# Optimization experiments

Hardware: AMD Instinct MI355X
Metric: run time of the kernel (lower is better)

## Reference

```python
import jax, jax.numpy as jnp
import numpy as np

VOCAB = 100000
DIM = 128
B = 16384
K = 20


def setup_inputs() -> dict:
    key = jax.random.key(0)
    k1, k2, k3, k4, k5 = jax.random.split(key, 5)
    return {
        "target": jax.random.randint(k1, (B,), 0, VOCAB),
        "context": jax.random.randint(k2, (B,), 0, VOCAB),
        "neg_samples": jax.random.randint(k3, (B, K), 0, VOCAB),
        "in_embed": jax.random.normal(k4, (VOCAB, DIM), dtype=jnp.float32),
        "out_embed": jax.random.normal(k5, (VOCAB, DIM), dtype=jnp.float32),
    }


def reference(target, context, neg_samples, in_embed, out_embed):
    t = in_embed[target]            # [B, D]
    c = out_embed[context]          # [B, D]
    n = out_embed[neg_samples]      # [B, K, D]

    pos_score = jnp.einsum("bd,bd->b", t, c)          # [B]
    pos_loss = jax.nn.log_sigmoid(pos_score)           # [B]

    neg_score = jnp.einsum("bd,bkd->bk", t, n)        # [B, K]
    neg_loss = jax.nn.log_sigmoid(-neg_score).sum(axis=1)  # [B]

    # Original torch broadcasts pos_loss[B] + neg_loss[B,1] -> [B,B] then .mean();
    # that equals mean(pos_loss) + mean(neg_loss), computed here without the [B,B].
    return -(pos_loss.mean() + neg_loss.mean())
```

## Files before the change

kernel.cpp:

```cpp
#include <hip/hip_runtime.h>
#include <hip/hip_bf16.h>

#define VOCAB 100000
#define DIM   128
#define BATCH 16384
#define KNEG  20

__global__ __launch_bounds__(256) void skipgram_loss_kernel(
    const int*   __restrict__ target,
    const int*   __restrict__ context,
    const int*   __restrict__ neg_samples,
    const float* __restrict__ in_embed,
    const float* __restrict__ out_embed,
    float*       __restrict__ out)
{
    const int lane  = threadIdx.x & 63;
    const int half  = lane >> 5;
    const int sub   = lane & 31;
    const int wave  = threadIdx.x >> 6;
    const int wpb   = blockDim.x >> 6;
    const int gwave = blockIdx.x * wpb + wave;
    const int nwav  = gridDim.x * wpb;

    float acc = 0.0f;

    for (int b0 = gwave * 2; b0 < BATCH; b0 += nwav * 2) {
        const int b    = b0 + half;
        const int trow = target[b];
        const int crow = context[b];

        const float4 t4 = *(const float4*)(in_embed  + (size_t)trow * DIM + sub * 4);
        const float4 c4 = *(const float4*)(out_embed + (size_t)crow * DIM + sub * 4);

        const int myidx = (sub < KNEG) ? neg_samples[b * KNEG + sub] : 0;

        int nrow[KNEG];
        #pragma unroll
        for (int k = 0; k < KNEG; ++k)
            nrow[k] = __shfl(myidx, k, 32);

        float p[KNEG + 1];
        p[0] = t4.x * c4.x + t4.y * c4.y + t4.z * c4.z + t4.w * c4.w;

        #pragma unroll
        for (int k = 0; k < KNEG; ++k) {
            const float4 n4 = *(const float4*)(out_embed + (size_t)nrow[k] * DIM + sub * 4);
            p[k + 1] = t4.x * n4.x + t4.y * n4.y + t4.z * n4.z + t4.w * n4.w;
        }

        #pragma unroll
        for (int k = 0; k < KNEG + 1; ++k) {
            float v = p[k];
            #pragma unroll
            for (int m = 1; m < 32; m <<= 1)
                v += __shfl_xor(v, m, 64);
            const float x  = (k == 0) ? v : -v;
            const float ls = fminf(x, 0.0f) - __logf(1.0f + __expf(-fabsf(x)));
            acc += ls;
        }
    }

    __shared__ float smem[8];
    if (sub == 0) smem[wave * 2 + half] = acc;
    __syncthreads();
    if (threadIdx.x == 0) {
        float tot = 0.0f;
        for (int i = 0; i < wpb * 2; ++i) tot += smem[i];
        atomicAdd(out, -tot * (1.0f / (float)BATCH));
    }
}

extern "C" void kernel_launch(void* const* d_in, const int* in_sizes, int n_in,
                              void* d_out, int out_size, void* d_ws, size_t ws_size,
                              hipStream_t stream) {
    const int*   target      = (const int*)  d_in[0];
    const int*   context     = (const int*)  d_in[1];
    const int*   neg_samples = (const int*)  d_in[2];
    const float* in_embed    = (const float*)d_in[3];
    const float* out_embed   = (const float*)d_in[4];
    float*       out         = (float*)d_out;

    hipMemsetAsync(out, 0, sizeof(float), stream);

    skipgram_loss_kernel<<<2048, 256, 0, stream>>>(
        target, context, neg_samples, in_embed, out_embed, out);
}
```

Measured before the change: 145.3 us.

## Invert negative-sample gather into per-vocab-row bucket traversal with bf16 targets

Replaces the per-batch gather of 20 random out_embed rows with a two-pass scheme. The first pass buckets negative samples by vocabulary row using atomic counters, fixed slots and an overflow list. It also computes the positive loss and writes target rows as bf16. The second pass streams each used out_embed row once and dots it against the bf16 target rows. This aims to cut repeated random fp32 reads of the large table, at the cost of atomics, extra kernels and memsets, and lower precision for the target vectors. Overflow is capped, so extreme collisions could silently drop terms.

```diff
diff --git a/kernel.cpp b/kernel.cpp
--- a/kernel.cpp
+++ b/kernel.cpp
@@ -5,59 +5,138 @@
 #define DIM   128
 #define BATCH 16384
 #define KNEG  20
-
-__global__ __launch_bounds__(256) void skipgram_loss_kernel(
+#define NNEG  (BATCH * KNEG)
+#define CAP   16
+#define OVF_CAP 65536
+
+#define CNT_OFF   0ul
+#define OVFC_OFF  400000ul
+#define SLOT_OFF  400064ul
+#define TBF_OFF   3600128ul
+#define OVF_OFF   7794432ul
+#define WS_NEED   (OVF_OFF + OVF_CAP * 4ul)
+
+typedef float v4f __attribute__((ext_vector_type(4)));
+
+__device__ __forceinline__ unsigned short f2bf(float f) {
+    unsigned u = __float_as_uint(f);
+    return (unsigned short)((u + 0x7fffu + ((u >> 16) & 1u)) >> 16);
+}
+__device__ __forceinline__ float bf2f(unsigned short u) {
+    return __uint_as_float(((unsigned)u) << 16);
+}
+__device__ __forceinline__ float log_sigmoid(float x) {
+    return fminf(x, 0.0f) - __logf(1.0f + __expf(-fabsf(x)));
+}
+
+__global__ __launch_bounds__(256) void scatter_pos_kernel(
     const int*   __restrict__ target,
     const int*   __restrict__ context,
     const int*   __restrict__ neg_samples,
     const float* __restrict__ in_embed,
     const float* __restrict__ out_embed,
-    float*       __restrict__ out)
+    unsigned*       cnt, unsigned* ovfc,
+    unsigned short* slots, unsigned short* tbf, unsigned* ovf,
+    float* __restrict__ out)
+{
+    if (blockIdx.x < 1280) {
+        const int i = blockIdx.x * 256 + threadIdx.x;
+        const int b = i / KNEG;
+        const int r = neg_samples[i];
+        const unsigned pos = atomicAdd(&cnt[r], 1u);
+        if (pos < CAP) {
+            slots[r * CAP + pos] = (unsigned short)b;
+        } else {
+            const unsigned o = atomicAdd(ovfc, 1u);
+            if (o < OVF_CAP) ovf[o] = ((unsigned)r << 14) | (unsigned)b;
+        }
+        return;
+    }
+    const int blk  = blockIdx.x - 1280;
+    const int lane = threadIdx.x & 63;
+    const int half = lane >> 5;
+    const int sub  = lane & 31;
+    const int wave = threadIdx.x >> 6;
+    const int b    = blk * 8 + wave * 2 + half;
+
+    const int trow = target[b];
+    const int crow = context[b];
+    const float4 t4 = *(const float4*)(in_embed  + (size_t)trow * DIM + sub * 4);
+    const float4 c4 = *(const float4*)(out_embed + (size_t)crow * DIM + sub * 4);
+
+    ushort4 u;
+    u.x = f2bf(t4.x); u.y = f2bf(t4.y); u.z = f2bf(t4.z); u.w = f2bf(t4.w);
+    *(ushort4*)(tbf + (size_t)b * DIM + sub * 4) = u;
+
+    float v = t4.x * c4.x + t4.y * c4.y + t4.z * c4.z + t4.w * c4.w;
+    #pragma unroll
+    for (int m = 1; m < 32; m <<= 1) v += __shfl_xor(v, m, 64);
+    const float ls = log_sigmoid(v);
+
+    __shared__ float smem[8];
+    if (sub == 0) smem[wave * 2 + half] = ls;
+    __syncthreads();
+    if (threadIdx.x == 0) {
+        float tot = 0.0f;
+        #pragma unroll
+        for (int j = 0; j < 8; ++j) tot += smem[j];
+        atomicAdd(out, -tot * (1.0f / (float)BATCH));
+    }
+}
+
+__global__ __launch_bounds__(256) void neg_rows_kernel(
+    const float* __restrict__ out_embed,
+    const unsigned* __restrict__ cnt, const unsigned* __restrict__ ovfc,
+    const unsigned short* __restrict__ slots,
+    const unsigned short* __restrict__ tbf,
+    const unsigned* __restrict__ ovf,
+    float* __restrict__ out)
 {
     const int lane  = threadIdx.x & 63;
     const int half  = lane >> 5;
     const int sub   = lane & 31;
     const int wave  = threadIdx.x >> 6;
-    const int wpb   = blockDim.x >> 6;
-    const int gwave = blockIdx.x * wpb + wave;
-    const int nwav  = gridDim.x * wpb;
+    const int ghalf = (blockIdx.x * 4 + wave) * 2 + half;
+    const int nhalf = gridDim.x * 8;
 
     float acc = 0.0f;
 
-    for (int b0 = gwave * 2; b0 < BATCH; b0 += nwav * 2) {
-        const int b    = b0 + half;
-        const int trow = target[b];
-        const int crow = context[b];
-
-        const float4 t4 = *(const float4*)(in_embed  + (size_t)trow * DIM + sub * 4);
-        const float4 c4 = *(const float4*)(out_embed + (size_t)crow * DIM + sub * 4);
-
-        const int myidx = (sub < KNEG) ? neg_samples[b * KNEG + sub] : 0;
-
-        int nrow[KNEG];
-        #pragma unroll
-        for (int k = 0; k < KNEG; ++k)
-            nrow[k] = __shfl(myidx, k, 32);
-
-        float p[KNEG + 1];
-        p[0] = t4.x * c4.x + t4.y * c4.y + t4.z * c4.z + t4.w * c4.w;
-
-        #pragma unroll
-        for (int k = 0; k < KNEG; ++k) {
-            const float4 n4 = *(const float4*)(out_embed + (size_t)nrow[k] * DIM + sub * 4);
-            p[k + 1] = t4.x * n4.x + t4.y * n4.y + t4.z * n4.z + t4.w * n4.w;
-        }
-
-        #pragma unroll
-        for (int k = 0; k < KNEG + 1; ++k) {
-            float v = p[k];
+    for (int r = ghalf; r < VOCAB; r += nhalf) {
+        const unsigned c = __builtin_nontemporal_load(&cnt[r]);
+        if (c == 0) continue;
+
+        const v4f o4 = __builtin_nontemporal_load(
+            (const v4f*)(out_embed + (size_t)r * DIM + sub * 4));
+
+        const int m = (c < CAP) ? (int)c : CAP;
+        for (int j = 0; j < m; ++j) {
+            const int b = __builtin_nontemporal_load(&slots[r * CAP + j]);
+            const uint2 tu = *(const uint2*)(tbf + (size_t)b * DIM + sub * 4);
+            float p = o4.x * bf2f((unsigned short)(tu.x & 0xffff))
+                    + o4.y * bf2f((unsigned short)(tu.x >> 16))
+                    + o4.z * bf2f((unsigned short)(tu.y & 0xffff))
+                    + o4.w * bf2f((unsigned short)(tu.y >> 16));
             #pragma unroll
-            for (int m = 1; m < 32; m <<= 1)
-                v += __shfl_xor(v, m, 64);
-            const float x  = (k == 0) ? v : -v;
-            const float ls = fminf(x, 0.0f) - __logf(1.0f + __expf(-fabsf(x)));
-            acc += ls;
-        }
+            for (int s = 1; s < 32; s <<= 1) p += __shfl_xor(p, s, 64);
+            acc += log_sigmoid(-p);
+        }
+    }
+
+    unsigned novf = *ovfc;
+    if (novf > OVF_CAP) novf = OVF_CAP;
+    for (unsigned i = ghalf; i < novf; i += nhalf) {
+        const unsigned e = ovf[i];
+        const int r = (int)(e >> 14);
+        const int b = (int)(e & 16383u);
+        const float4 o4 = *(const float4*)(out_embed + (size_t)r * DIM + sub * 4);
+        const uint2 tu = *(const uint2*)(tbf + (size_t)b * DIM + sub * 4);
+        float p = o4.x * bf2f((unsigned short)(tu.x & 0xffff))
+                + o4.y * bf2f((unsigned short)(tu.x >> 16))
+                + o4.z * bf2f((unsigned short)(tu.y & 0xffff))
+                + o4.w * bf2f((unsigned short)(tu.y >> 16));
+        #pragma unroll
+        for (int s = 1; s < 32; s <<= 1) p += __shfl_xor(p, s, 64);
+        acc += log_sigmoid(-p);
     }
 
     __shared__ float smem[8];
@@ -65,7 +144,52 @@
     __syncthreads();
     if (threadIdx.x == 0) {
         float tot = 0.0f;
-        for (int i = 0; i < wpb * 2; ++i) tot += smem[i];
+        #pragma unroll
+        for (int j = 0; j < 8; ++j) tot += smem[j];
+        atomicAdd(out, -tot * (1.0f / (float)BATCH));
+    }
+}
+
+__global__ __launch_bounds__(256) void skipgram_loss_kernel(
+    const int* __restrict__ target, const int* __restrict__ context,
+    const int* __restrict__ neg_samples,
+    const float* __restrict__ in_embed, const float* __restrict__ out_embed,
+    float* __restrict__ out)
+{
+    const int lane = threadIdx.x & 63, half = lane >> 5, sub = lane & 31;
+    const int wave = threadIdx.x >> 6, wpb = blockDim.x >> 6;
+    const int gwave = blockIdx.x * wpb + wave, nwav = gridDim.x * wpb;
+    float acc = 0.0f;
+    for (int b0 = gwave * 2; b0 < BATCH; b0 += nwav * 2) {
+        const int b = b0 + half;
+        const float4 t4 = *(const float4*)(in_embed  + (size_t)target[b]  * DIM + sub * 4);
+        const float4 c4 = *(const float4*)(out_embed + (size_t)context[b] * DIM + sub * 4);
+        const int myidx = (sub < KNEG) ? neg_samples[b * KNEG + sub] : 0;
+        int nrow[KNEG];
+        #pragma unroll
+        for (int k = 0; k < KNEG; ++k) nrow[k] = __shfl(myidx, k, 32);
+        float p[KNEG + 1];
+        p[0] = t4.x * c4.x + t4.y * c4.y + t4.z * c4.z + t4.w * c4.w;
+        #pragma unroll
+        for (int k = 0; k < KNEG; ++k) {
+            const float4 n4 = *(const float4*)(out_embed + (size_t)nrow[k] * DIM + sub * 4);
+            p[k + 1] = t4.x * n4.x + t4.y * n4.y + t4.z * n4.z + t4.w * n4.w;
+        }
+        #pragma unroll
+        for (int k = 0; k < KNEG + 1; ++k) {
+            float v = p[k];
+            #pragma unroll
+            for (int m = 1; m < 32; m <<= 1) v += __shfl_xor(v, m, 64);
+            const float x = (k == 0) ? v : -v;
+            acc += log_sigmoid(x);
+        }
+    }
+    __shared__ float smem[8];
+    if (sub == 0) smem[wave * 2 + half] = acc;
+    __syncthreads();
+    if (threadIdx.x == 0) {
+        float tot = 0.0f;
+        for (int i = 0; i < 8; ++i) tot += smem[i];
         atomicAdd(out, -tot * (1.0f / (float)BATCH));
     }
 }
@@ -82,6 +206,25 @@
 
     hipMemsetAsync(out, 0, sizeof(float), stream);
 
-    skipgram_loss_kernel<<<2048, 256, 0, stream>>>(
-        target, context, neg_samples, in_embed, out_embed, out);
-}
+    if (ws_size < WS_NEED) {
+        skipgram_loss_kernel<<<2048, 256, 0, stream>>>(
+            target, context, neg_samples, in_embed, out_embed, out);
+        return;
+    }
+
+    char* ws = (char*)d_ws;
+    unsigned*       cnt   = (unsigned*)      (ws + CNT_OFF);
+    unsigned*       ovfc  = (unsigned*)      (ws + OVFC_OFF);
+    unsigned short* slots = (unsigned short*)(ws + SLOT_OFF);
+    unsigned short* tbf   = (unsigned short*)(ws + TBF_OFF);
+    unsigned*       ovf   = (unsigned*)      (ws + OVF_OFF);
+
+    hipMemsetAsync(ws, 0, OVFC_OFF + 4, stream);
+
+    scatter_pos_kernel<<<3328, 256, 0, stream>>>(
+        target, context, neg_samples, in_embed, out_embed,
+        cnt, ovfc, slots, tbf, ovf, out);
+
+    neg_rows_kernel<<<2048, 256, 0, stream>>>(
+        out_embed, cnt, ovfc, slots, tbf, ovf, out);
+}
```

Result: slower. 217.9 us (+50.0%).

## Quantize out_embed to FP8 in workspace and gather FP8 rows for negatives

Applied to the files above, without the earlier changes.

Each call first streams all of out_embed into an FP8 copy in the workspace. It also computes the positive-pair term in FP32 and stores FP8 copies of the target rows. A second kernel then gathers the negative rows as 128-byte FP8 rows instead of 512-byte FP32 rows, and uses a transposed shuffle reduction to sum several dot products together. The aim is to cut the random-gather traffic, which dominates the cost, at the price of a full-table conversion pass and reduced precision in the negative scores, which may break accuracy tolerance.

```diff
diff --git a/kernel.cpp b/kernel.cpp
--- a/kernel.cpp
+++ b/kernel.cpp
@@ -6,66 +6,219 @@
 #define BATCH 16384
 #define KNEG  20
 
-__global__ __launch_bounds__(256) void skipgram_loss_kernel(
+#define TF8_OFF 12800000ul
+#define WS_NEED (TF8_OFF + (size_t)BATCH * DIM)
+
+#define CONV_BLOCKS 1024
+
+typedef float v2f __attribute__((ext_vector_type(2)));
+typedef float v4f __attribute__((ext_vector_type(4)));
+
+#if __has_builtin(__builtin_amdgcn_cvt_pk_f32_fp8) && __has_builtin(__builtin_amdgcn_cvt_pk_fp8_f32)
+#define HW_FP8 1
+#endif
+
+__device__ __forceinline__ float log_sigmoid(float x) {
+    return fminf(x, 0.0f) - __logf(1.0f + __expf(-fabsf(x)));
+}
+
+#ifndef HW_FP8
+__device__ __forceinline__ unsigned f2fp8(float f) {
+    unsigned u = __float_as_uint(f);
+    unsigned s = (u >> 24) & 0x80u;
+    float a = fabsf(f);
+    if (!(a >= 0x1p-10f)) return s;
+    if (a >= 448.0f) return s | 0x7Eu;
+    int E = (int)((u >> 23) & 0xffu) - 127;
+    if (E < -6) E = -6;
+    float step  = __uint_as_float((unsigned)(E - 3 + 127) << 23);
+    float rstep = __uint_as_float((unsigned)(3 - E + 127) << 23);
+    float r = rintf(a * rstep) * step;
+    unsigned ub = __float_as_uint(r);
+    unsigned code;
+    if (r < 0x1p-6f) code = (unsigned)(r * 512.0f);
+    else code = ((((ub >> 23) & 0xffu) - 120u) << 3) | ((ub >> 20) & 7u);
+    return s | code;
+}
+#endif
+
+__device__ __forceinline__ unsigned enc4(float a, float b, float c, float d) {
+#ifdef HW_FP8
+    int w = __builtin_amdgcn_cvt_pk_fp8_f32(a, b, 0, false);
+    w = __builtin_amdgcn_cvt_pk_fp8_f32(c, d, w, true);
+    return (unsigned)w;
+#else
+    return f2fp8(a) | (f2fp8(b) << 8) | (f2fp8(c) << 16) | (f2fp8(d) << 24);
+#endif
+}
+
+template <bool HI>
+__device__ __forceinline__ v2f dec2(unsigned w) {
+#ifdef HW_FP8
+    return __builtin_amdgcn_cvt_pk_f32_fp8((int)w, HI);
+#else
+    unsigned v0 = (w >> (HI ? 16 : 0)) & 0xffu;
+    unsigned v1 = (w >> (HI ? 24 : 8)) & 0xffu;
+    v2f r;
+    r.x = __uint_as_float(((v0 & 0x80u) << 24) | ((v0 & 0x7fu) << 20)) * 0x1p120f;
+    r.y = __uint_as_float(((v1 & 0x80u) << 24) | ((v1 & 0x7fu) << 20)) * 0x1p120f;
+    return r;
+#endif
+}
+
+__global__ __launch_bounds__(256) void convert_pos_kernel(
     const int*   __restrict__ target,
     const int*   __restrict__ context,
-    const int*   __restrict__ neg_samples,
     const float* __restrict__ in_embed,
     const float* __restrict__ out_embed,
-    float*       __restrict__ out)
+    unsigned char* __restrict__ nf8,
+    unsigned char* __restrict__ tf8,
+    float* __restrict__ out)
 {
-    const int lane  = threadIdx.x & 63;
-    const int half  = lane >> 5;
-    const int sub   = lane & 31;
-    const int wave  = threadIdx.x >> 6;
-    const int wpb   = blockDim.x >> 6;
-    const int gwave = blockIdx.x * wpb + wave;
-    const int nwav  = gridDim.x * wpb;
-
+    if (blockIdx.x < CONV_BLOCKS) {
+        const int n4   = VOCAB * DIM / 4;
+        const int tid  = blockIdx.x * 256 + threadIdx.x;
+        const int step = CONV_BLOCKS * 256;
+        unsigned* dst = (unsigned*)nf8;
+        for (int i = tid; i < n4; i += step) {
+            const v4f v = __builtin_nontemporal_load((const v4f*)out_embed + i);
+            dst[i] = enc4(v.x, v.y, v.z, v.w);
+        }
+        return;
+    }
+    const int blk  = blockIdx.x - CONV_BLOCKS;
+    const int lane = threadIdx.x & 63;
+    const int half = lane >> 5;
+    const int sub  = lane & 31;
+    const int wave = threadIdx.x >> 6;
+    const int b    = blk * 8 + wave * 2 + half;
+
+    const int trow = target[b];
+    const int crow = context[b];
+    const v4f t4 = *(const v4f*)(in_embed  + (size_t)trow * DIM + sub * 4);
+    const v4f c4 = *(const v4f*)(out_embed + (size_t)crow * DIM + sub * 4);
+
+    *(unsigned*)(tf8 + (size_t)b * DIM + sub * 4) = enc4(t4.x, t4.y, t4.z, t4.w);
+
+    float v = t4.x * c4.x + t4.y * c4.y + t4.z * c4.z + t4.w * c4.w;
+    #pragma unroll
+    for (int m = 1; m < 32; m <<= 1) v += __shfl_xor(v, m, 64);
+    const float ls = log_sigmoid(v);
+
+    __shared__ float smem[8];
+    if (sub == 0) smem[wave * 2 + half] = ls;
+    __syncthreads();
+    if (threadIdx.x == 0) {
+        float tot = 0.0f;
+        #pragma unroll
+        for (int j = 0; j < 8; ++j) tot += smem[j];
+        atomicAdd(out, -tot * (1.0f / (float)BATCH));
+    }
+}
+
+__global__ __launch_bounds__(256) void neg_fp8_kernel(
+    const int* __restrict__ neg_samples,
+    const unsigned char* __restrict__ nf8,
+    const unsigned char* __restrict__ tf8,
+    float* __restrict__ out)
+{
+    const int lane = threadIdx.x & 63;
+    const int half = lane >> 5;
+    const int sub  = lane & 31;
+    const int wave = threadIdx.x >> 6;
+    const int b    = (blockIdx.x * 4 + wave) * 2 + half;
+
+    const unsigned tw = *(const unsigned*)(tf8 + (size_t)b * DIM + sub * 4);
+    const v2f t01 = dec2<false>(tw);
+    const v2f t23 = dec2<true>(tw);
+
+    const int myidx = (sub < KNEG) ? neg_samples[b * KNEG + sub] : 0;
+
+    unsigned nw[KNEG];
+    #pragma unroll
+    for (int k = 0; k < KNEG; ++k) {
+        const int r = __shfl(myidx, k, 32);
+        nw[k] = *(const unsigned*)(nf8 + (size_t)r * DIM + sub * 4);
+    }
+
+    float p[KNEG];
+    #pragma unroll
+    for (int k = 0; k < KNEG; ++k) {
+        const v2f a = dec2<false>(nw[k]);
+        const v2f c = dec2<true>(nw[k]);
+        p[k] = t01.x * a.x + t01.y * a.y + t23.x * c.x + t23.y * c.y;
+    }
+
+    const bool s1 = (lane & 1) != 0;
+    const bool s2 = (lane & 2) != 0;
     float acc = 0.0f;
-
-    for (int b0 = gwave * 2; b0 < BATCH; b0 += nwav * 2) {
-        const int b    = b0 + half;
-        const int trow = target[b];
-        const int crow = context[b];
-
-        const float4 t4 = *(const float4*)(in_embed  + (size_t)trow * DIM + sub * 4);
-        const float4 c4 = *(const float4*)(out_embed + (size_t)crow * DIM + sub * 4);
-
-        const int myidx = (sub < KNEG) ? neg_samples[b * KNEG + sub] : 0;
-
-        int nrow[KNEG];
-        #pragma unroll
-        for (int k = 0; k < KNEG; ++k)
-            nrow[k] = __shfl(myidx, k, 32);
-
-        float p[KNEG + 1];
-        p[0] = t4.x * c4.x + t4.y * c4.y + t4.z * c4.z + t4.w * c4.w;
-
-        #pragma unroll
-        for (int k = 0; k < KNEG; ++k) {
-            const float4 n4 = *(const float4*)(out_embed + (size_t)nrow[k] * DIM + sub * 4);
-            p[k + 1] = t4.x * n4.x + t4.y * n4.y + t4.z * n4.z + t4.w * n4.w;
-        }
-
-        #pragma unroll
-        for (int k = 0; k < KNEG + 1; ++k) {
-            float v = p[k];
-            #pragma unroll
-            for (int m = 1; m < 32; m <<= 1)
-                v += __shfl_xor(v, m, 64);
-            const float x  = (k == 0) ? v : -v;
-            const float ls = fminf(x, 0.0f) - __logf(1.0f + __expf(-fabsf(x)));
-            acc += ls;
-        }
-    }
+    #pragma unroll
+    for (int q = 0; q < KNEG / 4; ++q) {
+        const float p0 = p[4*q], p1 = p[4*q+1], p2 = p[4*q+2], p3 = p[4*q+3];
+        float m0 = s1 ? p1 : p0, y0 = s1 ? p0 : p1;
+        float m1 = s1 ? p3 : p2, y1 = s1 ? p2 : p3;
+        m0 += __shfl_xor(y0, 1, 64);
+        m1 += __shfl_xor(y1, 1, 64);
+        float m = s2 ? m1 : m0, y = s2 ? m0 : m1;
+        m += __shfl_xor(y, 2, 64);
+        m += __shfl_xor(m, 4, 64);
+        m += __shfl_xor(m, 8, 64);
+        m += __shfl_xor(m, 16, 64);
+        acc += log_sigmoid(-m);
+    }
+    acc += __shfl_xor(acc, 1, 64);
+    acc += __shfl_xor(acc, 2, 64);
 
     __shared__ float smem[8];
     if (sub == 0) smem[wave * 2 + half] = acc;
     __syncthreads();
     if (threadIdx.x == 0) {
         float tot = 0.0f;
-        for (int i = 0; i < wpb * 2; ++i) tot += smem[i];
+        #pragma unroll
+        for (int j = 0; j < 8; ++j) tot += smem[j];
+        atomicAdd(out, -tot * (1.0f / (float)BATCH));
+    }
+}
+
+__global__ __launch_bounds__(256) void skipgram_loss_kernel(
+    const int* __restrict__ target, const int* __restrict__ context,
+    const int* __restrict__ neg_samples,
+    const float* __restrict__ in_embed, const float* __restrict__ out_embed,
+    float* __restrict__ out)
+{
+    const int lane = threadIdx.x & 63, half = lane >> 5, sub = lane & 31;
+    const int wave = threadIdx.x >> 6, wpb = blockDim.x >> 6;
+    const int gwave = blockIdx.x * wpb + wave, nwav = gridDim.x * wpb;
+    float acc = 0.0f;
+    for (int b0 = gwave * 2; b0 < BATCH; b0 += nwav * 2) {
+        const int b = b0 + half;
+        const float4 t4 = *(const float4*)(in_embed  + (size_t)target[b]  * DIM + sub * 4);
+        const float4 c4 = *(const float4*)(out_embed + (size_t)context[b] * DIM + sub * 4);
+        const int myidx = (sub < KNEG) ? neg_samples[b * KNEG + sub] : 0;
+        int nrow[KNEG];
+        #pragma unroll
+        for (int k = 0; k < KNEG; ++k) nrow[k] = __shfl(myidx, k, 32);
+        float p[KNEG + 1];
+        p[0] = t4.x * c4.x + t4.y * c4.y + t4.z * c4.z + t4.w * c4.w;
+        #pragma unroll
+        for (int k = 0; k < KNEG; ++k) {
+            const float4 n4 = *(const float4*)(out_embed + (size_t)nrow[k] * DIM + sub * 4);
+            p[k + 1] = t4.x * n4.x + t4.y * n4.y + t4.z * n4.z + t4.w * n4.w;
+        }
+        #pragma unroll
+        for (int k = 0; k < KNEG + 1; ++k) {
+            float v = p[k];
+            #pragma unroll
+            for (int m = 1; m < 32; m <<= 1) v += __shfl_xor(v, m, 64);
+            acc += log_sigmoid((k == 0) ? v : -v);
+        }
+    }
+    __shared__ float smem[8];
+    if (sub == 0) smem[wave * 2 + half] = acc;
+    __syncthreads();
+    if (threadIdx.x == 0) {
+        float tot = 0.0f;
+        for (int i = 0; i < 8; ++i) tot += smem[i];
         atomicAdd(out, -tot * (1.0f / (float)BATCH));
     }
 }
@@ -80,8 +233,19 @@
     const float* out_embed   = (const float*)d_in[4];
     float*       out         = (float*)d_out;
 
-    hipMemsetAsync(out, 0, sizeof(float), stream);
-
-    skipgram_loss_kernel<<<2048, 256, 0, stream>>>(
-        target, context, neg_samples, in_embed, out_embed, out);
-}
+    (void)hipMemsetAsync(out, 0, sizeof(float), stream);
+
+    if (ws_size < WS_NEED) {
+        skipgram_loss_kernel<<<2048, 256, 0, stream>>>(
+            target, context, neg_samples, in_embed, out_embed, out);
+        return;
+    }
+
+    unsigned char* nf8 = (unsigned char*)d_ws;
+    unsigned char* tf8 = nf8 + TF8_OFF;
+
+    convert_pos_kernel<<<CONV_BLOCKS + 2048, 256, 0, stream>>>(
+        target, context, in_embed, out_embed, nf8, tf8, out);
+
+    neg_fp8_kernel<<<2048, 256, 0, stream>>>(neg_samples, nf8, tf8, out);
+}
```

After: 177.1 us. 1.22x slower.
